# Kernel optimization log

Hardware: AMD Instinct MI355X
Metric: run time of the kernel (lower is better)

Reference implementation:

```python
import jax, jax.numpy as jnp
import numpy as np

B, N, DIM = 4, 2048, 512
HEADS, DIM_HEAD = 8, 64
INNER = HEADS * DIM_HEAD  # == DIM, so to_out is Identity
LN_EPS = 1e-5
MASK_FILL = 1e-8  # faithful to torch.where(mask, attn, 1e-08)


def setup_inputs() -> dict:
    key = jax.random.key(0)
    k1, k2 = jax.random.split(key)
    x = jax.random.normal(k1, (B, N, DIM), dtype=jnp.float32)
    gamma = jnp.ones((DIM,), dtype=jnp.float32)
    beta = jnp.zeros((DIM,), dtype=jnp.float32)
    w_qkv = jax.random.normal(k2, (3 * INNER, DIM), dtype=jnp.float32) * (DIM ** -0.5)
    mask = jnp.tril(jnp.ones((N, N), dtype=bool))  # causal boolean mask, asserted 2-D in source
    return {"x": x, "gamma": gamma, "beta": beta, "w_qkv": w_qkv, "mask": mask}


def reference(x, gamma, beta, w_qkv, mask):
    # LayerNorm over last dim
    mu = jnp.mean(x, axis=-1, keepdims=True)
    var = jnp.var(x, axis=-1, keepdims=True)
    h = (x - mu) * jax.lax.rsqrt(var + LN_EPS) * gamma + beta
    # qkv projection (no bias), chunk into q, k, v
    qkv = h @ w_qkv.T  # [B, N, 3*INNER]
    q, k, v = jnp.split(qkv, 3, axis=-1)

    def to_heads(t):  # b n (h d) -> b h n d
        return t.reshape(B, N, HEADS, DIM_HEAD).transpose(0, 2, 1, 3)

    q, k, v = to_heads(q), to_heads(k), to_heads(v)
    # NOTE: original forward does NOT apply self.scale
    attn = jnp.einsum('bhnd,bhmd->bhnm', q, k)
    attn = jnp.where(mask[None, None, :, :], attn, MASK_FILL)
    p = jax.nn.softmax(attn, axis=-1)
    out = jnp.einsum('bhnm,bhmd->bhnd', p, v)
    out = out.transpose(0, 2, 1, 3).reshape(B, N, INNER)  # b h n d -> b n (h d)
    return out  # to_out is Identity since INNER == DIM
```

## Files before the change

kernel.cpp:

```cpp
#include <hip/hip_runtime.h>
#include <hip/hip_bf16.h>
#include <math.h>

#define B_  4
#define N_  2048
#define DIM_ 512
#define HEADS_ 8
#define QKV_ 1536
#define MASK_C 1e-8f
#define M_FIX 12.0f
#define LOG2E 1.44269504f

typedef __bf16 bf16_t;
typedef bf16_t bf16x8 __attribute__((ext_vector_type(8)));
typedef float  f32x4  __attribute__((ext_vector_type(4)));

__device__ __forceinline__ bf16_t f2b(float x) { return (bf16_t)x; }
__device__ __forceinline__ float  b2f(bf16_t x) { return (float)x; }

__device__ __forceinline__ f32x4 mfma16(bf16x8 a, bf16x8 b, f32x4 c) {
    return __builtin_amdgcn_mfma_f32_16x16x32_bf16(a, b, c, 0, 0, 0);
}

__global__ __launch_bounds__(256) void ln_wsplit_kernel(const float* __restrict__ x,
                                                        const float* __restrict__ gamma,
                                                        const float* __restrict__ beta,
                                                        bf16_t* __restrict__ hh,
                                                        bf16_t* __restrict__ hl,
                                                        const float* __restrict__ wq,
                                                        bf16_t* __restrict__ wh,
                                                        bf16_t* __restrict__ wl) {
    int blk = blockIdx.x;
    int t = threadIdx.x;
    if (blk >= B_ * N_) {
        int i = ((blk - B_ * N_) * 256 + t) * 4;
        float4 v = *(const float4*)&wq[i];
        float vv[4] = {v.x, v.y, v.z, v.w};
        #pragma unroll
        for (int j = 0; j < 4; j++) {
            bf16_t hi = f2b(vv[j]);
            wh[i + j] = hi;
            wl[i + j] = f2b(vv[j] - b2f(hi));
        }
        return;
    }
    int row = blk;
    const float* xr = x + (size_t)row * DIM_;
    float2 xv = *(const float2*)&xr[2 * t];
    float e0 = xv.x, e1 = xv.y;
    float s  = e0 + e1;
    float sq = e0 * e0 + e1 * e1;
    for (int off = 32; off; off >>= 1) {
        s  += __shfl_xor(s, off);
        sq += __shfl_xor(sq, off);
    }
    __shared__ float red[8];
    int w = t >> 6;
    if ((t & 63) == 0) { red[w] = s; red[4 + w] = sq; }
    __syncthreads();
    float S  = red[0] + red[1] + red[2] + red[3];
    float SQ = red[4] + red[5] + red[6] + red[7];
    float mu = S * (1.0f / DIM_);
    float var = SQ * (1.0f / DIM_) - mu * mu;
    float rs = rsqrtf(var + 1e-5f);
    float2 gv = *(const float2*)&gamma[2 * t];
    float2 bv = *(const float2*)&beta[2 * t];
    float y0 = (e0 - mu) * rs * gv.x + bv.x;
    float y1 = (e1 - mu) * rs * gv.y + bv.y;
    size_t base = (size_t)row * DIM_ + 2 * t;
    bf16_t h0 = f2b(y0), h1 = f2b(y1);
    __align__(4) bf16_t hp[2] = {h0, h1};
    __align__(4) bf16_t lp[2] = {f2b(y0 - b2f(h0)), f2b(y1 - b2f(h1))};
    *(unsigned int*)&hh[base] = *(unsigned int*)hp;
    *(unsigned int*)&hl[base] = *(unsigned int*)lp;
}

__global__ __launch_bounds__(256, 3) void qkv_gemm(const bf16_t* __restrict__ hh,
                                                   const bf16_t* __restrict__ hl,
                                                   const bf16_t* __restrict__ wh,
                                                   const bf16_t* __restrict__ wl,
                                                   bf16_t* __restrict__ qh, bf16_t* __restrict__ ql,
                                                   bf16_t* __restrict__ kh, bf16_t* __restrict__ kl,
                                                   bf16_t* __restrict__ vth,
                                                   float* __restrict__ part) {
    __shared__ __align__(16) bf16_t smem[20480];
    bf16_t* Ah = smem;
    bf16_t* Al = smem + 5120;
    bf16_t* Bh = smem + 10240;
    bf16_t* Bl = smem + 15360;
    int bm = blockIdx.x & 63;
    int bn = blockIdx.x >> 6;
    int t = threadIdx.x;
    int w = t >> 6, lane = t & 63, quad = lane >> 4, l16 = lane & 15;

    f32x4 acc[2][8];
    #pragma unroll
    for (int i = 0; i < 2; i++)
        #pragma unroll
        for (int j = 0; j < 8; j++) acc[i][j] = (f32x4)(0.0f);

    int sr = t >> 1, skc = (t & 1) * 16;
    size_t gA = (size_t)(bm * 128 + sr) * 512 + skc;
    size_t gB = (size_t)(bn * 128 + sr) * 512 + skc;

    uint4 rAh0 = *(const uint4*)&hh[gA];
    uint4 rAh1 = *(const uint4*)&hh[gA + 8];
    uint4 rAl0 = *(const uint4*)&hl[gA];
    uint4 rAl1 = *(const uint4*)&hl[gA + 8];
    uint4 rBh0 = *(const uint4*)&wh[gB];
    uint4 rBh1 = *(const uint4*)&wh[gB + 8];
    uint4 rBl0 = *(const uint4*)&wl[gB];
    uint4 rBl1 = *(const uint4*)&wl[gB + 8];

    for (int k0 = 0; k0 < 512; k0 += 32) {
        __syncthreads();
        *(uint4*)&Ah[sr * 40 + skc]     = rAh0;
        *(uint4*)&Ah[sr * 40 + skc + 8] = rAh1;
        *(uint4*)&Al[sr * 40 + skc]     = rAl0;
        *(uint4*)&Al[sr * 40 + skc + 8] = rAl1;
        *(uint4*)&Bh[sr * 40 + skc]     = rBh0;
        *(uint4*)&Bh[sr * 40 + skc + 8] = rBh1;
        *(uint4*)&Bl[sr * 40 + skc]     = rBl0;
        *(uint4*)&Bl[sr * 40 + skc + 8] = rBl1;
        __syncthreads();

        if (k0 < 480) {
            int kn = k0 + 32;
            rAh0 = *(const uint4*)&hh[gA + kn];
            rAh1 = *(const uint4*)&hh[gA + kn + 8];
            rAl0 = *(const uint4*)&hl[gA + kn];
            rAl1 = *(const uint4*)&hl[gA + kn + 8];
            rBh0 = *(const uint4*)&wh[gB + kn];
            rBh1 = *(const uint4*)&wh[gB + kn + 8];
            rBl0 = *(const uint4*)&wl[gB + kn];
            rBl1 = *(const uint4*)&wl[gB + kn + 8];
        }

        bf16x8 aH[2], aL[2];
        #pragma unroll
        for (int mt = 0; mt < 2; mt++) {
            aH[mt] = *(const bf16x8*)&Ah[(w * 32 + mt * 16 + l16) * 40 + quad * 8];
            aL[mt] = *(const bf16x8*)&Al[(w * 32 + mt * 16 + l16) * 40 + quad * 8];
        }
        #pragma unroll
        for (int nt = 0; nt < 8; nt++) {
            bf16x8 bH = *(const bf16x8*)&Bh[(nt * 16 + l16) * 40 + quad * 8];
            bf16x8 bL = *(const bf16x8*)&Bl[(nt * 16 + l16) * 40 + quad * 8];
            #pragma unroll
            for (int mt = 0; mt < 2; mt++) {
                acc[mt][nt] = mfma16(aH[mt], bH, acc[mt][nt]);
                acc[mt][nt] = mfma16(aH[mt], bL, acc[mt][nt]);
                acc[mt][nt] = mfma16(aL[mt], bH, acc[mt][nt]);
            }
        }
    }

    if (bn < 8) {
        bf16_t* dsth = (bn < 4) ? qh : kh;
        bf16_t* dstl = (bn < 4) ? ql : kl;
        int ncol0 = (bn & 3) * 128 + (t & 15) * 8;
        int r0 = t >> 4;
        #pragma unroll
        for (int pass = 0; pass < 2; pass++) {
            __syncthreads();
            #pragma unroll
            for (int mt = 0; mt < 2; mt++)
                #pragma unroll
                for (int nt = 0; nt < 8; nt++)
                    #pragma unroll
                    for (int reg = 0; reg < 4; reg++) {
                        float v = acc[mt][nt][reg];
                        bf16_t hi = f2b(v);
                        bf16_t val = pass ? f2b(v - b2f(hi)) : hi;
                        smem[(w * 32 + mt * 16 + quad * 4 + reg) * 132 + nt * 16 + l16] = val;
                    }
            __syncthreads();
            bf16_t* dst = pass ? dstl : dsth;
            #pragma unroll
            for (int i = 0; i < 8; i++) {
                int row = r0 + i * 16;
                *(uint4*)&dst[(size_t)(bm * 128 + row) * 512 + ncol0] =
                    *(const uint4*)&smem[row * 132 + ((t & 15) * 8)];
            }
        }
    } else {
        int bb = bm >> 4, key0 = (bm & 15) * 128;
        int n = t & 127, mc = (t >> 7) * 64;
        int head = (bn - 8) * 2 + (n >> 6), dd = n & 63;
        size_t obase = ((size_t)((bb * 8 + head) * 64 + dd)) * 2048 + key0 + mc;
        float Ssum = 0.0f;
        #pragma unroll
        for (int pass = 0; pass < 2; pass++) {
            __syncthreads();
            #pragma unroll
            for (int mt = 0; mt < 2; mt++)
                #pragma unroll
                for (int nt = 0; nt < 8; nt++)
                    #pragma unroll
                    for (int reg = 0; reg < 4; reg++) {
                        float v = acc[mt][nt][reg];
                        bf16_t hi = f2b(v);
                        bf16_t val = pass ? f2b(v - b2f(hi)) : hi;
                        smem[(w * 32 + mt * 16 + quad * 4 + reg) * 132 + nt * 16 + l16] = val;
                    }
            __syncthreads();
            #pragma unroll
            for (int i = 0; i < 64; i += 8) {
                __align__(16) bf16_t v8[8];
                #pragma unroll
                for (int j = 0; j < 8; j++) {
                    v8[j] = smem[(mc + i + j) * 132 + n];
                    Ssum += b2f(v8[j]);
                }
                if (pass == 0)
                    *(uint4*)&vth[obase + i] = *(const uint4*)v8;
            }
        }
        int tt = (key0 >> 6) + (mc >> 6);
        part[((size_t)((bb * 8 + head) * 32 + tt)) * 64 + dd] = Ssum;
    }
}

__global__ __launch_bounds__(256, 4) void attn_kernel(const bf16_t* __restrict__ qh,
                                                      const bf16_t* __restrict__ ql,
                                                      const bf16_t* __restrict__ kh,
                                                      const bf16_t* __restrict__ kl,
                                                      const bf16_t* __restrict__ vth,
                                                      const float* __restrict__ part,
                                                      float* __restrict__ out) {
    __shared__ __align__(16) bf16_t smem[17152];
    __shared__ float sufl[4][64];
    char* lds = (char*)smem;
    bf16_t* Ps = smem + 12288;

    int blk = blockIdx.x;
    int bh = blk & 31;
    int gi = blk >> 5;
    int g3 = gi & 7;
    int q4 = gi >> 3;
    int rt;
    if (q4 == 0)      rt = 31 - g3;
    else if (q4 == 1) rt = g3;
    else if (q4 == 2) rt = 23 - g3;
    else              rt = 8 + g3;
    int b = bh >> 3, head = bh & 7;
    int t = threadIdx.x;
    int w = t >> 6, lane = t & 63, quad = lane >> 4, l16 = lane & 15;

    {
        int d = t & 63, g = t >> 6;
        float s = 0.0f;
        for (int tt = rt + 1 + g; tt < 32; tt += 4)
            s += part[((size_t)bh * 32 + tt) * 64 + d];
        sufl[g][d] = s;
    }

    bf16x8 qAH[2], qAL[2];
    {
        int qrow = rt * 64 + w * 16 + l16;
        size_t g = ((size_t)(b * N_ + qrow)) * 512 + head * 64 + quad * 8;
        qAH[0] = *(const bf16x8*)&qh[g];
        qAH[1] = *(const bf16x8*)&qh[g + 32];
        qAL[0] = *(const bf16x8*)&ql[g];
        qAL[1] = *(const bf16x8*)&ql[g + 32];
    }
    bf16x8 ones;
    #pragma unroll
    for (int j = 0; j < 8; j++) ones[j] = f2b(1.0f);

    f32x4 O[4];
    #pragma unroll
    for (int nt = 0; nt < 4; nt++) O[nt] = (f32x4)(0.0f);
    f32x4 Lacc = (f32x4)(0.0f);
    const float mbias = M_FIX * LOG2E;

    int r = t >> 2, c16 = t & 3;
    int swz = (r & 7) << 4;
    int lk0 = r * 128 + ((c16 * 32)      ^ swz);
    int lk1 = r * 128 + ((c16 * 32 + 16) ^ swz);
    size_t gk = ((size_t)(b * N_ + r)) * 512 + head * 64 + c16 * 16;
    size_t gv = ((size_t)(bh * 64 + r)) * 2048 + c16 * 16;

    uint4 pKh0 = *(const uint4*)&kh[gk];
    uint4 pKh1 = *(const uint4*)&kh[gk + 8];
    uint4 pKl0 = *(const uint4*)&kl[gk];
    uint4 pKl1 = *(const uint4*)&kl[gk + 8];
    uint4 pVh0 = *(const uint4*)&vth[gv];
    uint4 pVh1 = *(const uint4*)&vth[gv + 8];

    for (int jt = 0; jt <= rt; jt++) {
        __syncthreads();
        *(uint4*)(lds + lk0)         = pKh0;
        *(uint4*)(lds + lk1)         = pKh1;
        *(uint4*)(lds + 8192 + lk0)  = pKl0;
        *(uint4*)(lds + 8192 + lk1)  = pKl1;
        *(uint4*)(lds + 16384 + lk0) = pVh0;
        *(uint4*)(lds + 16384 + lk1) = pVh1;
        __syncthreads();

        if (jt < rt) {
            gk += (size_t)64 * 512;
            gv += 64;
            pKh0 = *(const uint4*)&kh[gk];
            pKh1 = *(const uint4*)&kh[gk + 8];
            pKl0 = *(const uint4*)&kl[gk];
            pKl1 = *(const uint4*)&kl[gk + 8];
            pVh0 = *(const uint4*)&vth[gv];
            pVh1 = *(const uint4*)&vth[gv + 8];
        }

        f32x4 S[4];
        #pragma unroll
        for (int nt = 0; nt < 4; nt++) S[nt] = (f32x4)(0.0f);
        __builtin_amdgcn_s_setprio(1);
        #pragma unroll
        for (int khf = 0; khf < 2; khf++) {
            #pragma unroll
            for (int nt = 0; nt < 4; nt++) {
                int row = nt * 16 + l16;
                int bc = (khf * 64 + quad * 16) ^ ((row & 7) << 4);
                bf16x8 bH = *(const bf16x8*)(lds + row * 128 + bc);
                bf16x8 bL = *(const bf16x8*)(lds + 8192 + row * 128 + bc);
                S[nt] = mfma16(qAH[khf], bH, S[nt]);
                S[nt] = mfma16(qAH[khf], bL, S[nt]);
                S[nt] = mfma16(qAL[khf], bH, S[nt]);
            }
        }
        __builtin_amdgcn_s_setprio(0);

        if (jt == rt) {
            int lrow = w * 16 + quad * 4;
            #pragma unroll
            for (int nt = 0; nt < 4; nt++)
                #pragma unroll
                for (int reg = 0; reg < 4; reg++)
                    if (nt * 16 + l16 > lrow + reg) S[nt][reg] = MASK_C;
        }

        #pragma unroll
        for (int nt = 0; nt < 4; nt++)
            #pragma unroll
            for (int reg = 0; reg < 4; reg++)
                Ps[(w * 16 + quad * 4 + reg) * 76 + nt * 16 + l16] =
                    f2b(exp2f(fmaf(S[nt][reg], LOG2E, -mbias)));

        bf16x8 pH[2];
        #pragma unroll
        for (int khf = 0; khf < 2; khf++)
            pH[khf] = *(const bf16x8*)&Ps[(w * 16 + l16) * 76 + khf * 32 + quad * 8];

        __builtin_amdgcn_s_setprio(1);
        #pragma unroll
        for (int khf = 0; khf < 2; khf++) Lacc = mfma16(pH[khf], ones, Lacc);

        #pragma unroll
        for (int khf = 0; khf < 2; khf++) {
            #pragma unroll
            for (int nt = 0; nt < 4; nt++) {
                int row = nt * 16 + l16;
                int bc = (khf * 64 + quad * 16) ^ ((row & 7) << 4);
                bf16x8 vB = *(const bf16x8*)(lds + 16384 + row * 128 + bc);
                O[nt] = mfma16(pH[khf], vB, O[nt]);
            }
        }
        __builtin_amdgcn_s_setprio(0);
    }

    float L[4];
    #pragma unroll
    for (int reg = 0; reg < 4; reg++) L[reg] = Lacc[reg];
    int cnt = N_ - (rt + 1) * 64;
    if (cnt > 0) {
        float pc = expf(MASK_C - M_FIX);
        float sv[4];
        #pragma unroll
        for (int nt = 0; nt < 4; nt++) {
            int d = nt * 16 + l16;
            sv[nt] = sufl[0][d] + sufl[1][d] + sufl[2][d] + sufl[3][d];
        }
        #pragma unroll
        for (int reg = 0; reg < 4; reg++) {
            L[reg] += pc * (float)cnt;
            #pragma unroll
            for (int nt = 0; nt < 4; nt++) O[nt][reg] += pc * sv[nt];
        }
    }

    #pragma unroll
    for (int reg = 0; reg < 4; reg++) {
        float rl = 1.0f / L[reg];
        int row = rt * 64 + w * 16 + quad * 4 + reg;
        #pragma unroll
        for (int nt = 0; nt < 4; nt++)
            out[((size_t)(b * N_ + row)) * DIM_ + head * 64 + nt * 16 + l16] =
                O[nt][reg] * rl;
    }
}

extern "C" void kernel_launch(void* const* d_in, const int* in_sizes, int n_in,
                              void* d_out, int out_size, void* d_ws, size_t ws_size,
                              hipStream_t stream) {
    const float* x     = (const float*)d_in[0];
    const float* gamma = (const float*)d_in[1];
    const float* beta  = (const float*)d_in[2];
    const float* w_qkv = (const float*)d_in[3];
    float* out = (float*)d_out;

    const size_t HW = (size_t)8192 * 512;
    const size_t WN = (size_t)1536 * 512;
    bf16_t* hh  = (bf16_t*)d_ws;
    bf16_t* hl  = hh + HW;
    bf16_t* qh  = hl + HW;
    bf16_t* ql  = qh + HW;
    bf16_t* kh  = ql + HW;
    bf16_t* kl  = kh + HW;
    bf16_t* vth = kl + HW;
    bf16_t* vtl = vth + HW;
    bf16_t* wh  = vtl + HW;
    bf16_t* wl  = wh + WN;
    float*  part = (float*)(wl + WN);

    ln_wsplit_kernel<<<B_ * N_ + 768, 256, 0, stream>>>(x, gamma, beta, hh, hl,
                                                        w_qkv, wh, wl);
    qkv_gemm<<<768, 256, 0, stream>>>(hh, hl, wh, wl, qh, ql, kh, kl, vth, part);
    attn_kernel<<<1024, 256, 0, stream>>>(qh, ql, kh, kl, vth, part, out);
}
```

Baseline: 192.6 us.

## Software-pipeline attention loop with double-buffered K and triple-buffered V in LDS

Restructures the attention main loop so that the PV matmul for the previous key tile runs alongside the QK matmul for the current tile. K is double-buffered and V triple-buffered in LDS, so the next tile's stores happen after compute and only one barrier per iteration remains instead of two. This hides the softmax-to-PV dependency and cuts barrier stalls. In exchange LDS use grows to about 57KB per block, and occupancy is lowered to 2 blocks per CU through launch bounds.

```diff
diff --git a/kernel.cpp b/kernel.cpp
--- a/kernel.cpp
+++ b/kernel.cpp
@@ -221,17 +221,17 @@
     }
 }
 
-__global__ __launch_bounds__(256, 4) void attn_kernel(const bf16_t* __restrict__ qh,
+__global__ __launch_bounds__(256, 2) void attn_kernel(const bf16_t* __restrict__ qh,
                                                       const bf16_t* __restrict__ ql,
                                                       const bf16_t* __restrict__ kh,
                                                       const bf16_t* __restrict__ kl,
                                                       const bf16_t* __restrict__ vth,
                                                       const float* __restrict__ part,
                                                       float* __restrict__ out) {
-    __shared__ __align__(16) bf16_t smem[17152];
+    __shared__ __align__(16) bf16_t smem[28672];
+    __shared__ __align__(16) bf16_t Ps[4 * 16 * 76];
     __shared__ float sufl[4][64];
     char* lds = (char*)smem;
-    bf16_t* Ps = smem + 12288;
 
     int blk = blockIdx.x;
     int bh = blk & 31;
@@ -287,16 +287,20 @@
     uint4 pKl1 = *(const uint4*)&kl[gk + 8];
     uint4 pVh0 = *(const uint4*)&vth[gv];
     uint4 pVh1 = *(const uint4*)&vth[gv + 8];
+    *(uint4*)(lds + lk0)         = pKh0;
+    *(uint4*)(lds + lk1)         = pKh1;
+    *(uint4*)(lds + 8192 + lk0)  = pKl0;
+    *(uint4*)(lds + 8192 + lk1)  = pKl1;
+    *(uint4*)(lds + 32768 + lk0) = pVh0;
+    *(uint4*)(lds + 32768 + lk1) = pVh1;
+    __syncthreads();
+
+    bf16x8 pHp[2];
+    int vp = 0, vc = 0;
 
     for (int jt = 0; jt <= rt; jt++) {
-        __syncthreads();
-        *(uint4*)(lds + lk0)         = pKh0;
-        *(uint4*)(lds + lk1)         = pKh1;
-        *(uint4*)(lds + 8192 + lk0)  = pKl0;
-        *(uint4*)(lds + 8192 + lk1)  = pKl1;
-        *(uint4*)(lds + 16384 + lk0) = pVh0;
-        *(uint4*)(lds + 16384 + lk1) = pVh1;
-        __syncthreads();
+        int vn = (vc == 2) ? 0 : vc + 1;
+        char* kcur = lds + (jt & 1) * 16384;
 
         if (jt < rt) {
             gk += (size_t)64 * 512;
@@ -319,11 +323,27 @@
             for (int nt = 0; nt < 4; nt++) {
                 int row = nt * 16 + l16;
                 int bc = (khf * 64 + quad * 16) ^ ((row & 7) << 4);
-                bf16x8 bH = *(const bf16x8*)(lds + row * 128 + bc);
-                bf16x8 bL = *(const bf16x8*)(lds + 8192 + row * 128 + bc);
+                bf16x8 bH = *(const bf16x8*)(kcur + row * 128 + bc);
+                bf16x8 bL = *(const bf16x8*)(kcur + 8192 + row * 128 + bc);
                 S[nt] = mfma16(qAH[khf], bH, S[nt]);
                 S[nt] = mfma16(qAH[khf], bL, S[nt]);
                 S[nt] = mfma16(qAL[khf], bH, S[nt]);
+            }
+        }
+
+        if (jt > 0) {
+            #pragma unroll
+            for (int khf = 0; khf < 2; khf++) Lacc = mfma16(pHp[khf], ones, Lacc);
+            const char* vbp = lds + 32768 + vp * 8192;
+            #pragma unroll
+            for (int khf = 0; khf < 2; khf++) {
+                #pragma unroll
+                for (int nt = 0; nt < 4; nt++) {
+                    int row = nt * 16 + l16;
+                    int bc = (khf * 64 + quad * 16) ^ ((row & 7) << 4);
+                    bf16x8 vB = *(const bf16x8*)(vbp + row * 128 + bc);
+                    O[nt] = mfma16(pHp[khf], vB, O[nt]);
+                }
             }
         }
         __builtin_amdgcn_s_setprio(0);
@@ -344,23 +364,37 @@
                 Ps[(w * 16 + quad * 4 + reg) * 76 + nt * 16 + l16] =
                     f2b(exp2f(fmaf(S[nt][reg], LOG2E, -mbias)));
 
-        bf16x8 pH[2];
         #pragma unroll
         for (int khf = 0; khf < 2; khf++)
-            pH[khf] = *(const bf16x8*)&Ps[(w * 16 + l16) * 76 + khf * 32 + quad * 8];
-
+            pHp[khf] = *(const bf16x8*)&Ps[(w * 16 + l16) * 76 + khf * 32 + quad * 8];
+
+        if (jt < rt) {
+            char* kb = lds + ((jt + 1) & 1) * 16384;
+            char* vb = lds + 32768 + vn * 8192;
+            *(uint4*)(kb + lk0)        = pKh0;
+            *(uint4*)(kb + lk1)        = pKh1;
+            *(uint4*)(kb + 8192 + lk0) = pKl0;
+            *(uint4*)(kb + 8192 + lk1) = pKl1;
+            *(uint4*)(vb + lk0)        = pVh0;
+            *(uint4*)(vb + lk1)        = pVh1;
+        }
+        __syncthreads();
+        vp = vc; vc = vn;
+    }
+
+    {
         __builtin_amdgcn_s_setprio(1);
         #pragma unroll
-        for (int khf = 0; khf < 2; khf++) Lacc = mfma16(pH[khf], ones, Lacc);
-
+        for (int khf = 0; khf < 2; khf++) Lacc = mfma16(pHp[khf], ones, Lacc);
+        const char* vbp = lds + 32768 + vp * 8192;
         #pragma unroll
         for (int khf = 0; khf < 2; khf++) {
             #pragma unroll
             for (int nt = 0; nt < 4; nt++) {
                 int row = nt * 16 + l16;
                 int bc = (khf * 64 + quad * 16) ^ ((row & 7) << 4);
-                bf16x8 vB = *(const bf16x8*)(lds + 16384 + row * 128 + bc);
-                O[nt] = mfma16(pH[khf], vB, O[nt]);
+                bf16x8 vB = *(const bf16x8*)(vbp + row * 128 + bc);
+                O[nt] = mfma16(pHp[khf], vB, O[nt]);
             }
         }
         __builtin_amdgcn_s_setprio(0);
```

After: 198.8 us. 1.03x slower.
